# Optimization experiments

Hardware: AMD Instinct MI355X
Metric: run time of the kernel (lower is better)

Reference implementation:

```python
import jax, jax.numpy as jnp
import numpy as np

N = 50000
E = 640000
D_IN = 128
D_OUT = 128


def setup_inputs() -> dict:
    key = jax.random.key(0)
    k1, k2, k3, k4 = jax.random.split(key, 4)
    x = jax.random.normal(k1, (N, D_IN), dtype=jnp.float32)
    edge_index = jax.random.randint(k2, (2, E), 0, N, dtype=jnp.int64)
    # Linear(in_channels, out_channels) params, PyTorch default init scale
    lim = 1.0 / np.sqrt(D_IN)
    W = jax.random.uniform(k3, (D_IN, D_OUT), dtype=jnp.float32, minval=-lim, maxval=lim)
    b = jax.random.uniform(k4, (D_OUT,), dtype=jnp.float32, minval=-lim, maxval=lim)
    return {"x": x, "edge_index": edge_index, "W": W, "b": b}


def reference(x, edge_index, W, b):
    row, col = edge_index[0], edge_index[1]
    # gather source features, segment-sum onto destination rows
    msgs = x[col]  # [E, D_IN]
    summed = jax.ops.segment_sum(msgs, row, num_segments=N)  # [N, D_IN]
    counts = jax.ops.segment_sum(jnp.ones((E,), dtype=x.dtype), row, num_segments=N)
    # scatter_mean: empty segments -> 0 (avoid div by zero)
    x_agg = summed / jnp.maximum(counts, 1.0)[:, None]
    # Linear + ReLU
    return jax.nn.relu(x_agg @ W + b)
```

## Files before the change

### kernel.cpp

```cpp
#include <hip/hip_runtime.h>

#define NN 50000
#define DD 128
#define PAD 16
#define CAP 48
#define GEMM_BLOCKS 782

typedef __attribute__((ext_vector_type(8))) short bf16x8;
typedef __attribute__((ext_vector_type(4))) float f32x4;

static __device__ __forceinline__ unsigned short f2bf(float x) {
    unsigned int u = __float_as_uint(x);
    unsigned int r = (u + 0x7fffu + ((u >> 16) & 1u)) >> 16;
    return (unsigned short)r;
}

static __device__ __forceinline__ int swz(int byte) {
    return byte ^ (((byte >> 8) & 7) << 4);
}

__global__ void __launch_bounds__(256) zero_wt_kernel(
    int* __restrict__ pad, const float* __restrict__ W, unsigned short* __restrict__ Wt)
{
    if (blockIdx.x == 0) {
        for (int idx = threadIdx.x; idx < DD * DD; idx += 256) {
            int k = idx >> 7;
            int j = idx & 127;
            Wt[j * DD + k] = f2bf(W[idx]);
        }
    }
    int i = blockIdx.x * 256 + threadIdx.x;
    const int total = NN * PAD / 4;
    if (i < total) {
        reinterpret_cast<uint4*>(pad)[i] = make_uint4(0u, 0u, 0u, 0u);
    }
}

__global__ void __launch_bounds__(256) ticket_place_kernel(
    const int* __restrict__ row, const int* __restrict__ col,
    int* __restrict__ pad, unsigned short* __restrict__ slot, int E)
{
    int e = blockIdx.x * 256 + threadIdx.x;
    if (e < E) {
        int r = row[e];
        int t = atomicAdd(&pad[r * PAD], 1);
        if (t < CAP) slot[r * CAP + t] = (unsigned short)col[e];
    }
}

__global__ void __launch_bounds__(256) gemm_xw_kernel(
    const float* __restrict__ x,
    const unsigned short* __restrict__ Wt,
    unsigned short* __restrict__ y)
{
    __shared__ unsigned short w_lds[DD * DD];
    __shared__ unsigned short a_lds[64 * DD];

    const int tid = threadIdx.x;
    const int i0 = blockIdx.x * 64;

    {
        const uint4* src = reinterpret_cast<const uint4*>(Wt);
        #pragma unroll
        for (int it = 0; it < 8; ++it) {
            int idx = tid + it * 256;
            uint4 v = src[idx];
            *reinterpret_cast<uint4*>((char*)w_lds + swz(idx * 16)) = v;
        }
    }
    #pragma unroll
    for (int it = 0; it < 8; ++it) {
        int idx = tid + it * 256;
        int r = idx >> 5;
        int c4 = idx & 31;
        int grow = i0 + r;
        float4 v = make_float4(0.f, 0.f, 0.f, 0.f);
        if (grow < NN) v = reinterpret_cast<const float4*>(x + (size_t)grow * DD)[c4];
        ushort4 o;
        o.x = f2bf(v.x); o.y = f2bf(v.y); o.z = f2bf(v.z); o.w = f2bf(v.w);
        *reinterpret_cast<ushort4*>((char*)a_lds + swz(r * 256 + c4 * 8)) = o;
    }
    __syncthreads();

    const int wave = tid >> 6;
    const int l64 = tid & 63;
    const int lrow = l64 & 15;
    const int kgrp = l64 >> 4;

    bf16x8 afrag[4];
    #pragma unroll
    for (int s = 0; s < 4; ++s) {
        int byte = (wave * 16 + lrow) * 256 + (s * 32 + kgrp * 8) * 2;
        afrag[s] = *reinterpret_cast<const bf16x8*>((char*)a_lds + swz(byte));
    }

    f32x4 acc[8];
    #pragma unroll
    for (int t = 0; t < 8; ++t) acc[t] = (f32x4){0.f, 0.f, 0.f, 0.f};

    #pragma unroll
    for (int t = 0; t < 8; ++t) {
        #pragma unroll
        for (int s = 0; s < 4; ++s) {
            int byte = (t * 16 + lrow) * 256 + (s * 32 + kgrp * 8) * 2;
            bf16x8 bfrag = *reinterpret_cast<const bf16x8*>((char*)w_lds + swz(byte));
            acc[t] = __builtin_amdgcn_mfma_f32_16x16x32_bf16(afrag[s], bfrag, acc[t], 0, 0, 0);
        }
    }
    __syncthreads();

    #pragma unroll
    for (int t = 0; t < 8; ++t) {
        #pragma unroll
        for (int r = 0; r < 4; ++r) {
            int lr = wave * 16 + kgrp * 4 + r;
            int byte = lr * 256 + (t * 16 + lrow) * 2;
            *reinterpret_cast<unsigned short*>((char*)a_lds + swz(byte)) = f2bf(acc[t][r]);
        }
    }
    __syncthreads();

    {
        uint4* dst = reinterpret_cast<uint4*>(y) + (size_t)i0 * 16;
        #pragma unroll
        for (int it = 0; it < 4; ++it) {
            int idx = tid + it * 256;
            if (i0 + (idx >> 4) < NN) {
                uint4 v = *reinterpret_cast<const uint4*>((char*)a_lds + swz(idx * 16));
                dst[idx] = v;
            }
        }
    }
}

__global__ void __launch_bounds__(256) gather_out_kernel(
    const unsigned short* __restrict__ y,
    const int* __restrict__ pad,
    const unsigned short* __restrict__ slot,
    const float* __restrict__ bias,
    float* __restrict__ out)
{
    int node = blockIdx.x * 8 + (threadIdx.x >> 5);
    int lane = threadIdx.x & 31;
    int q = lane >> 3;
    int l8 = lane & 7;
    if (node >= NN) return;
    int cnt0 = pad[node * PAD];
    int cnt = min(cnt0, CAP);
    int start = node * CAP;
    int end = start + cnt;

    float acc[16];
    #pragma unroll
    for (int j = 0; j < 16; ++j) acc[j] = 0.f;

    for (int base = start; base < end; base += 32) {
        int cl = (base + lane < end) ? (int)slot[base + lane] : 0;
        int m = min(32, end - base);
        for (int ii = 0; ii < m; ii += 4) {
            int src = ii + q;
            int c = __shfl(cl, src, 32);
            if (src < m) {
                const uint4* yp = reinterpret_cast<const uint4*>(y + (size_t)c * DD) + 2 * l8;
                uint4 u0 = yp[0];
                uint4 u1 = yp[1];
                acc[0]  += __uint_as_float(u0.x << 16);
                acc[1]  += __uint_as_float(u0.x & 0xffff0000u);
                acc[2]  += __uint_as_float(u0.y << 16);
                acc[3]  += __uint_as_float(u0.y & 0xffff0000u);
                acc[4]  += __uint_as_float(u0.z << 16);
                acc[5]  += __uint_as_float(u0.z & 0xffff0000u);
                acc[6]  += __uint_as_float(u0.w << 16);
                acc[7]  += __uint_as_float(u0.w & 0xffff0000u);
                acc[8]  += __uint_as_float(u1.x << 16);
                acc[9]  += __uint_as_float(u1.x & 0xffff0000u);
                acc[10] += __uint_as_float(u1.y << 16);
                acc[11] += __uint_as_float(u1.y & 0xffff0000u);
                acc[12] += __uint_as_float(u1.z << 16);
                acc[13] += __uint_as_float(u1.z & 0xffff0000u);
                acc[14] += __uint_as_float(u1.w << 16);
                acc[15] += __uint_as_float(u1.w & 0xffff0000u);
            }
        }
    }
    #pragma unroll
    for (int j = 0; j < 16; ++j) {
        acc[j] += __shfl_xor(acc[j], 8, 32);
        acc[j] += __shfl_xor(acc[j], 16, 32);
    }

    float inv = 1.0f / fmaxf((float)cnt0, 1.0f);
    float4 bb = reinterpret_cast<const float4*>(bias)[4 * l8 + q];
    float4 o;
    o.x = fmaxf(acc[4 * q + 0] * inv + bb.x, 0.f);
    o.y = fmaxf(acc[4 * q + 1] * inv + bb.y, 0.f);
    o.z = fmaxf(acc[4 * q + 2] * inv + bb.z, 0.f);
    o.w = fmaxf(acc[4 * q + 3] * inv + bb.w, 0.f);
    reinterpret_cast<float4*>(out + (size_t)node * DD)[4 * l8 + q] = o;
}

__global__ void __launch_bounds__(256) wt_only_kernel(
    const float* __restrict__ W, unsigned short* __restrict__ Wt)
{
    for (int idx = threadIdx.x; idx < DD * DD; idx += 256) {
        int k = idx >> 7;
        int j = idx & 127;
        Wt[j * DD + k] = f2bf(W[idx]);
    }
}

__global__ void __launch_bounds__(256) scatter_atomic_kernel(
    const float* __restrict__ x,
    const int* __restrict__ row, const int* __restrict__ col,
    float* __restrict__ agg, int* __restrict__ counts, int E)
{
    int gid = blockIdx.x * blockDim.x + threadIdx.x;
    int group = gid >> 5;
    int lane = threadIdx.x & 31;
    int ngroups = (gridDim.x * blockDim.x) >> 5;
    for (int e = group; e < E; e += ngroups) {
        int r = row[e];
        int c = col[e];
        float4 v = reinterpret_cast<const float4*>(x + (size_t)c * DD)[lane];
        float* dst = agg + (size_t)r * DD + lane * 4;
        unsafeAtomicAdd(dst + 0, v.x);
        unsafeAtomicAdd(dst + 1, v.y);
        unsafeAtomicAdd(dst + 2, v.z);
        unsafeAtomicAdd(dst + 3, v.w);
        if (lane == 0) atomicAdd(counts + r, 1);
    }
}

__global__ void __launch_bounds__(256) gemm_fb_kernel(
    const float* __restrict__ agg,
    const int* __restrict__ counts,
    const unsigned short* __restrict__ Wt,
    const float* __restrict__ bias,
    float* __restrict__ out)
{
    __shared__ unsigned short w_lds[DD * DD];
    __shared__ unsigned short a_lds[64 * DD];
    __shared__ float b_lds[DD];

    const int tid = threadIdx.x;
    const int i0 = blockIdx.x * 64;

    {
        const uint4* src = reinterpret_cast<const uint4*>(Wt);
        #pragma unroll
        for (int it = 0; it < 8; ++it) {
            int idx = tid + it * 256;
            *reinterpret_cast<uint4*>((char*)w_lds + swz(idx * 16)) = src[idx];
        }
    }
    if (tid < DD) b_lds[tid] = bias[tid];

    #pragma unroll
    for (int it = 0; it < 8; ++it) {
        int idx = tid + it * 256;
        int r = idx >> 5;
        int c4 = idx & 31;
        int grow = i0 + r;
        float4 v = make_float4(0.f, 0.f, 0.f, 0.f);
        float inv = 0.f;
        if (grow < NN) {
            v = reinterpret_cast<const float4*>(agg + (size_t)grow * DD)[c4];
            inv = 1.0f / fmaxf((float)counts[grow], 1.0f);
        }
        ushort4 o;
        o.x = f2bf(v.x * inv); o.y = f2bf(v.y * inv);
        o.z = f2bf(v.z * inv); o.w = f2bf(v.w * inv);
        *reinterpret_cast<ushort4*>((char*)a_lds + swz(r * 256 + c4 * 8)) = o;
    }
    __syncthreads();

    const int wave = tid >> 6;
    const int l64 = tid & 63;
    const int lrow = l64 & 15;
    const int kgrp = l64 >> 4;

    bf16x8 afrag[4];
    #pragma unroll
    for (int s = 0; s < 4; ++s) {
        int byte = (wave * 16 + lrow) * 256 + (s * 32 + kgrp * 8) * 2;
        afrag[s] = *reinterpret_cast<const bf16x8*>((char*)a_lds + swz(byte));
    }

    f32x4 acc[8];
    #pragma unroll
    for (int t = 0; t < 8; ++t) acc[t] = (f32x4){0.f, 0.f, 0.f, 0.f};

    #pragma unroll
    for (int t = 0; t < 8; ++t) {
        #pragma unroll
        for (int s = 0; s < 4; ++s) {
            int byte = (t * 16 + lrow) * 256 + (s * 32 + kgrp * 8) * 2;
            bf16x8 bfrag = *reinterpret_cast<const bf16x8*>((char*)w_lds + swz(byte));
            acc[t] = __builtin_amdgcn_mfma_f32_16x16x32_bf16(afrag[s], bfrag, acc[t], 0, 0, 0);
        }
    }

    #pragma unroll
    for (int t = 0; t < 8; ++t) {
        int colj = t * 16 + lrow;
        float bbv = b_lds[colj];
        #pragma unroll
        for (int r = 0; r < 4; ++r) {
            int grow = i0 + wave * 16 + kgrp * 4 + r;
            if (grow < NN) {
                out[(size_t)grow * DD + colj] = fmaxf(acc[t][r] + bbv, 0.f);
            }
        }
    }
}

extern "C" void kernel_launch(void* const* d_in, const int* in_sizes, int n_in,
                              void* d_out, int out_size, void* d_ws, size_t ws_size,
                              hipStream_t stream) {
    const float* x  = (const float*)d_in[0];
    const int* ei   = (const int*)d_in[1];
    const float* W  = (const float*)d_in[2];
    const float* b  = (const float*)d_in[3];
    float* out      = (float*)d_out;

    const int E = in_sizes[1] / 2;
    const int* row = ei;
    const int* col = ei + E;

    char* wsc = (char*)d_ws;
    int* pad             = (int*)(wsc + 0);
    unsigned short* slot = (unsigned short*)(wsc + 3200000);
    unsigned short* Wt   = (unsigned short*)(wsc + 8000000);
    unsigned short* y    = (unsigned short*)(wsc + 8032768);
    const size_t WS_NEED = 20832768;

    const int EB = (E + 255) / 256;

    if (ws_size >= WS_NEED) {
        zero_wt_kernel<<<800, 256, 0, stream>>>(pad, W, Wt);
        ticket_place_kernel<<<EB, 256, 0, stream>>>(row, col, pad, slot, E);
        gemm_xw_kernel<<<GEMM_BLOCKS, 256, 0, stream>>>(x, Wt, y);
        gather_out_kernel<<<(NN + 7) / 8, 256, 0, stream>>>(y, pad, slot, b, out);
    } else {
        int* fc = (int*)d_ws;
        unsigned short* fWt = (unsigned short*)(wsc + 200704);
        hipMemsetAsync(d_out, 0, (size_t)NN * DD * sizeof(float), stream);
        hipMemsetAsync(fc, 0, (size_t)NN * sizeof(int), stream);
        wt_only_kernel<<<1, 256, 0, stream>>>(W, fWt);
        scatter_atomic_kernel<<<2048, 256, 0, stream>>>(x, row, col, out, fc, E);
        gemm_fb_kernel<<<(NN + 63) / 64, 256, 0, stream>>>(out, fc, fWt, b, out);
    }
}
```

Measured before the change: 94.17 us.

## Load GEMM A fragments directly from global and double block tile size

The GEMM kernel now uses 512-thread blocks covering 128 rows, so the W tile staged in LDS is shared by twice as many rows and half as many blocks reload it. The A operand is read straight from global memory into MFMA fragment registers and converted to bf16 there, skipping the LDS staging pass and one barrier. The cost is less coalesced x reads (each lane reads 32-byte pieces across rows), and out-of-range rows are clamped to the last row instead of zero-filled. The GEMM is one of four kernels, so the effect on total time is bounded.

```diff
diff --git a/kernel.cpp b/kernel.cpp
--- a/kernel.cpp
+++ b/kernel.cpp
@@ -4,7 +4,7 @@
 #define DD 128
 #define PAD 16
 #define CAP 48
-#define GEMM_BLOCKS 782
+#define GEMM_BLOCKS 391
 
 typedef __attribute__((ext_vector_type(8))) short bf16x8;
 typedef __attribute__((ext_vector_type(4))) float f32x4;
@@ -48,51 +48,48 @@
     }
 }
 
-__global__ void __launch_bounds__(256) gemm_xw_kernel(
+__global__ void __launch_bounds__(512) gemm_xw_kernel(
     const float* __restrict__ x,
     const unsigned short* __restrict__ Wt,
     unsigned short* __restrict__ y)
 {
     __shared__ unsigned short w_lds[DD * DD];
-    __shared__ unsigned short a_lds[64 * DD];
+    __shared__ unsigned short r_lds[128 * DD];
 
     const int tid = threadIdx.x;
-    const int i0 = blockIdx.x * 64;
+    const int i0 = blockIdx.x * 128;
 
     {
         const uint4* src = reinterpret_cast<const uint4*>(Wt);
         #pragma unroll
-        for (int it = 0; it < 8; ++it) {
-            int idx = tid + it * 256;
+        for (int it = 0; it < 4; ++it) {
+            int idx = tid + it * 512;
             uint4 v = src[idx];
             *reinterpret_cast<uint4*>((char*)w_lds + swz(idx * 16)) = v;
         }
     }
-    #pragma unroll
-    for (int it = 0; it < 8; ++it) {
-        int idx = tid + it * 256;
-        int r = idx >> 5;
-        int c4 = idx & 31;
-        int grow = i0 + r;
-        float4 v = make_float4(0.f, 0.f, 0.f, 0.f);
-        if (grow < NN) v = reinterpret_cast<const float4*>(x + (size_t)grow * DD)[c4];
-        ushort4 o;
-        o.x = f2bf(v.x); o.y = f2bf(v.y); o.z = f2bf(v.z); o.w = f2bf(v.w);
-        *reinterpret_cast<ushort4*>((char*)a_lds + swz(r * 256 + c4 * 8)) = o;
-    }
-    __syncthreads();
 
     const int wave = tid >> 6;
     const int l64 = tid & 63;
     const int lrow = l64 & 15;
     const int kgrp = l64 >> 4;
+    const int grow = min(i0 + wave * 16 + lrow, NN - 1);
 
     bf16x8 afrag[4];
     #pragma unroll
     for (int s = 0; s < 4; ++s) {
-        int byte = (wave * 16 + lrow) * 256 + (s * 32 + kgrp * 8) * 2;
-        afrag[s] = *reinterpret_cast<const bf16x8*>((char*)a_lds + swz(byte));
-    }
+        const float4* xp = reinterpret_cast<const float4*>(
+            x + (size_t)grow * DD + s * 32 + kgrp * 8);
+        float4 p0 = xp[0];
+        float4 p1 = xp[1];
+        bf16x8 a;
+        a[0] = (short)f2bf(p0.x); a[1] = (short)f2bf(p0.y);
+        a[2] = (short)f2bf(p0.z); a[3] = (short)f2bf(p0.w);
+        a[4] = (short)f2bf(p1.x); a[5] = (short)f2bf(p1.y);
+        a[6] = (short)f2bf(p1.z); a[7] = (short)f2bf(p1.w);
+        afrag[s] = a;
+    }
+    __syncthreads();
 
     f32x4 acc[8];
     #pragma unroll
@@ -107,7 +104,6 @@
             acc[t] = __builtin_amdgcn_mfma_f32_16x16x32_bf16(afrag[s], bfrag, acc[t], 0, 0, 0);
         }
     }
-    __syncthreads();
 
     #pragma unroll
     for (int t = 0; t < 8; ++t) {
@@ -115,7 +111,7 @@
         for (int r = 0; r < 4; ++r) {
             int lr = wave * 16 + kgrp * 4 + r;
             int byte = lr * 256 + (t * 16 + lrow) * 2;
-            *reinterpret_cast<unsigned short*>((char*)a_lds + swz(byte)) = f2bf(acc[t][r]);
+            *reinterpret_cast<unsigned short*>((char*)r_lds + swz(byte)) = f2bf(acc[t][r]);
         }
     }
     __syncthreads();
@@ -124,9 +120,9 @@
         uint4* dst = reinterpret_cast<uint4*>(y) + (size_t)i0 * 16;
         #pragma unroll
         for (int it = 0; it < 4; ++it) {
-            int idx = tid + it * 256;
+            int idx = tid + it * 512;
             if (i0 + (idx >> 4) < NN) {
-                uint4 v = *reinterpret_cast<const uint4*>((char*)a_lds + swz(idx * 16));
+                uint4 v = *reinterpret_cast<const uint4*>((char*)r_lds + swz(idx * 16));
                 dst[idx] = v;
             }
         }
@@ -339,7 +335,7 @@
     if (ws_size >= WS_NEED) {
         zero_wt_kernel<<<800, 256, 0, stream>>>(pad, W, Wt);
         ticket_place_kernel<<<EB, 256, 0, stream>>>(row, col, pad, slot, E);
-        gemm_xw_kernel<<<GEMM_BLOCKS, 256, 0, stream>>>(x, Wt, y);
+        gemm_xw_kernel<<<GEMM_BLOCKS, 512, 0, stream>>>(x, Wt, y);
         gather_out_kernel<<<(NN + 7) / 8, 256, 0, stream>>>(y, pad, slot, b, out);
     } else {
         int* fc = (int*)d_ws;
```

Result: no change. 92.85 us (-1.4%).
